# Kernel optimization log

Hardware: AMD Instinct MI355X
Metric: run time of the kernel (lower is better)

## Reference

```python
import jax, jax.numpy as jnp
import numpy as np

N_NODES = 50000
IN_CH = 128
N_EDGES = 800000
ADD_CONST = 0.5


def setup_inputs() -> dict:
    key = jax.random.key(0)
    k1, k2, k3, k4, k5 = jax.random.split(key, 5)
    x = jax.random.normal(k1, (N_NODES, IN_CH), dtype=jnp.float32)
    edge_index = jax.random.randint(k2, (2, N_EDGES), 0, N_NODES, dtype=jnp.int32)
    edge_weight = jax.random.uniform(k3, (N_EDGES,), dtype=jnp.float32)
    # Linear(2*C -> 1): split into source/target halves (mathematically identical
    # to Linear on concat([x[row], x[col]])). Xavier-uniform-ish scale.
    lim = float(np.sqrt(6.0 / (2 * IN_CH + 1)))
    w_src = jax.random.uniform(k4, (IN_CH,), minval=-lim, maxval=lim, dtype=jnp.float32)
    w_dst = jax.random.uniform(k5, (IN_CH,), minval=-lim, maxval=lim, dtype=jnp.float32)
    b = jnp.zeros((), dtype=jnp.float32)
    return {"x": x, "w_src": w_src, "w_dst": w_dst, "b": b,
            "edge_index": edge_index, "edge_weight": edge_weight}


def _normalize_edge_score(score, row, num_nodes):
    """Per-source-node softmax over strictly-positive scores, +0.5; nodes with
    no positive incident edge keep raw scores (faithful to torch loop)."""
    pos = score > 0
    has_pos = jax.ops.segment_max(pos.astype(jnp.int32), row, num_segments=num_nodes) > 0
    neg_big = jnp.asarray(jnp.finfo(score.dtype).min, score.dtype)
    smax = jax.ops.segment_max(jnp.where(pos, score, neg_big), row, num_segments=num_nodes)
    safe_max = jnp.where(has_pos, smax, 0.0)
    exp_s = jnp.where(pos, jnp.exp(score - safe_max[row]), 0.0)
    denom = jax.ops.segment_sum(exp_s, row, num_segments=num_nodes)
    denom = jnp.where(denom > 0, denom, 1.0)
    soft = jnp.where(pos, exp_s / denom[row] + ADD_CONST, 0.0)
    return jnp.where(has_pos[row], soft, score)


def reference(x, w_src, w_dst, b, edge_index, edge_weight):
    N = x.shape[0]
    row, col = edge_index[0], edge_index[1]

    # Edge score: Linear on concat([x[row], x[col]]) == per-node projections gathered.
    score = (x @ w_src)[row] + (x @ w_dst)[col] + b          # [E]
    norm = _normalize_edge_score(score, row, N)              # [E]

    # Greedy contraction in descending score order. Because the torch loop skips
    # any edge whose endpoint cluster already has size > 1, this is exactly a
    # greedy maximal matching: carry only a per-node 'matched' bitmask.
    perm = jnp.argsort(-norm)
    r_s, c_s, s_s = row[perm], col[perm], norm[perm]

    def step(matched, uv):
        u, v = uv
        ok = (u != v) & ~matched[u] & ~matched[v]
        matched = matched.at[u].set(matched[u] | ok)
        matched = matched.at[v].set(matched[v] | ok)
        return matched, ok

    _, sel = jax.lax.scan(step, jnp.zeros((N,), dtype=bool), (r_s, c_s))  # sel: [E]

    # cluster[v] = u for each selected edge (u, v); everything else identity.
    drop_v = jnp.where(sel, c_s, N)   # out-of-range indices are dropped
    drop_u = jnp.where(sel, r_s, N)
    cluster = jnp.arange(N, dtype=jnp.int32).at[drop_v].set(r_s, mode='drop')
    s_rep = jnp.ones((N,), x.dtype).at[drop_u].set(s_s, mode='drop')       # score of merging edge at rep u
    partner = jnp.arange(N, dtype=jnp.int32).at[drop_u].set(c_s, mode='drop')
    rep_sel = jnp.zeros((N,), bool).at[drop_u].set(True, mode='drop')

    # torch: merged_x[u] = (x[u] + x[v]) * s ; merged_x[v] stays x[v];
    # new_x = index_add by cluster  =>  rep u gets (x[u]+x[v])*s + x[v].
    sum_x = jax.ops.segment_sum(x, cluster, num_segments=N)               # [N, C]
    new_x = sum_x * s_rep[:, None] + jnp.where(rep_sel[:, None], x[partner], 0.0)

    counts = jax.ops.segment_sum(jnp.ones((N,), jnp.int32), cluster, num_segments=N)
    is_rep = counts > 0          # rows of new_x that correspond to surviving clusters

    # Remap edges to cluster representatives; self-loops masked out.
    new_row = cluster[row]
    new_col = cluster[col]
    edge_valid = new_row != new_col

    return new_x, cluster, is_rep, new_row, new_col, edge_valid, edge_weight
```

## Files before the change

kernel.cpp:

```cpp
#include <hip/hip_runtime.h>
#include <cmath>

#define IN_CH 128
#define NBUCK 128
#define LNMAX 392
#define PLW(p) __hip_atomic_load((p), __ATOMIC_RELAXED, __HIP_MEMORY_SCOPE_WORKGROUP)

typedef unsigned long long ull;
typedef ull  ull2 __attribute__((ext_vector_type(2)));
typedef float f4  __attribute__((ext_vector_type(4)));

__device__ __forceinline__ ull make_key(float norm, int e) {
    unsigned int b = __float_as_uint(norm);
    unsigned int asc = (b & 0x80000000u) ? ~b : (b | 0x80000000u);
    unsigned int desc = ~asc;
    return (((ull)desc) << 32) | (unsigned int)e;
}

__global__ void proj_kernel(const float* __restrict__ x, const float* __restrict__ w_src,
                            const float* __restrict__ w_dst, float* __restrict__ p,
                            float* __restrict__ q,
                            ull* __restrict__ wsuit,
                            int* __restrict__ cluster, int* __restrict__ partner,
                            float* __restrict__ s_rep, int* __restrict__ bump,
                            int* __restrict__ btail, int N) {
    int gtid = blockIdx.x * blockDim.x + threadIdx.x;
    if (gtid == 0) *bump = 0;
    if (gtid < NBUCK) btail[gtid] = 0;
    if (gtid < N) {
        wsuit[gtid]    = ~0ULL;
        cluster[gtid]  = gtid;
        partner[gtid]  = gtid;
        s_rep[gtid]    = 1.0f;
    }
    int wave = gtid >> 6;
    int lane = threadIdx.x & 63;
    if (wave >= N) return;
    float2 xv = ((const float2*)(x + (size_t)wave * IN_CH))[lane];
    float2 ws = ((const float2*)w_src)[lane];
    float2 wd = ((const float2*)w_dst)[lane];
    double ap = (double)xv.x * (double)ws.x + (double)xv.y * (double)ws.y;
    double aq = (double)xv.x * (double)wd.x + (double)xv.y * (double)wd.y;
    #pragma unroll
    for (int off = 32; off > 0; off >>= 1) {
        ap += __shfl_down(ap, off);
        aq += __shfl_down(aq, off);
    }
    if (lane == 0) { p[wave] = (float)ap; q[wave] = (float)aq; }
}

__global__ void score_kernel(const int* __restrict__ row, const int* __restrict__ col,
                             const float* __restrict__ p, const float* __restrict__ q,
                             const float* __restrict__ bptr, float* __restrict__ score,
                             int2* __restrict__ rc, int* __restrict__ btail,
                             unsigned int* __restrict__ bucket, int bcap, int E) {
    __shared__ int cnt[NBUCK];
    __shared__ int gbase[NBUCK];
    int e = blockIdx.x * blockDim.x + threadIdx.x;
    if (threadIdx.x < NBUCK) cnt[threadIdx.x] = 0;
    __syncthreads();
    bool inb = e < E;
    int u = 0, v = 0, l1 = -1, l2 = -1, h1 = 0, h2 = 0;
    unsigned int selfbit = 0;
    if (inb) {
        u = row[e]; v = col[e];
        rc[e] = make_int2(u, v);
        float s = p[u] + q[v] + bptr[0];
        score[e] = s;
        selfbit = (u == v) ? (1u << 30) : 0u;
        h1 = u & (NBUCK - 1); l1 = atomicAdd(&cnt[h1], 1);
        if (u != v) {
            h2 = v & (NBUCK - 1); l2 = atomicAdd(&cnt[h2], 1);
        }
    }
    __syncthreads();
    if (threadIdx.x < NBUCK) gbase[threadIdx.x] = atomicAdd(&btail[threadIdx.x], cnt[threadIdx.x]);
    __syncthreads();
    if (l1 >= 0) bucket[(size_t)h1 * bcap + gbase[h1] + l1] =
        (unsigned int)e | ((unsigned int)(u >> 7) << 21) | selfbit;
    if (l2 >= 0) bucket[(size_t)h2 * bcap + gbase[h2] + l2] =
        (unsigned int)e | (1u << 20) | ((unsigned int)(v >> 7) << 21);
}

__global__ void slot_kernel(unsigned int* __restrict__ bucket, const int* __restrict__ btail,
                            int bcap, const float* __restrict__ score,
                            unsigned int* __restrict__ node_max, double* __restrict__ denom,
                            int* __restrict__ bump, int2* __restrict__ seg, int N) {
    __shared__ int hist[LNMAX];
    __shared__ unsigned int maxv[LNMAX];
    __shared__ double dden[LNMAX];
    __shared__ int scan[512];
    __shared__ int basesh;
    int b = blockIdx.x;
    int t = threadIdx.x;
    for (int i = t; i < LNMAX; i += blockDim.x) {
        hist[i] = 0; maxv[i] = 0u; dden[i] = 0.0;
    }
    __syncthreads();
    int n = btail[b];
    unsigned int* bk = bucket + (size_t)b * bcap;
    for (int i = t; i < n; i += blockDim.x) {
        unsigned int ent = bk[i];
        if (!(ent & (1u << 20))) {
            int e = (int)(ent & 0xfffffu);
            float s = score[e];
            if (s > 0.0f) {
                int ln = (int)((ent >> 21) & 0x1ffu);
                atomicMax(&maxv[ln], __float_as_uint(s));
            }
        }
    }
    __syncthreads();
    for (int i = t; i < n; i += blockDim.x) {
        unsigned int ent = bk[i];
        int ln = (int)((ent >> 21) & 0x1ffu);
        if (!(ent & (1u << 20))) {
            unsigned int mb = maxv[ln];
            int e = (int)(ent & 0xfffffu);
            float s = score[e];
            if (mb != 0u && s > 0.0f) {
                float m = __uint_as_float(mb);
                float ev = (float)exp((double)(s - m));
                atomicAdd(&dden[ln], (double)ev);
            }
        }
        if (ent & (1u << 30)) {
            bk[i] = 0xFFFFFFFFu;
        } else {
            int slot = atomicAdd(&hist[ln], 1);
            bk[i] = (ent & 0x1fffffu) | ((unsigned int)slot << 21);
        }
    }
    __syncthreads();
    int node = (t << 7) | b;
    int d  = (t < LNMAX && node < N) ? hist[t] : 0;
    int pd = (d + 3) & ~3;
    scan[t] = pd;
    __syncthreads();
    #pragma unroll
    for (int off = 1; off < 512; off <<= 1) {
        int add = (t >= off) ? scan[t - off] : 0;
        __syncthreads();
        scan[t] += add;
        __syncthreads();
    }
    if (t == 511) basesh = atomicAdd(bump, scan[511]);
    __syncthreads();
    if (t < LNMAX && node < N) {
        int lo = basesh + scan[t] - pd;
        seg[node]      = make_int2(lo, lo + d);
        node_max[node] = maxv[t];
        denom[node]    = dden[t];
    }
}

__global__ void norm_key_kernel(const int* __restrict__ row, const float* __restrict__ score,
                                const unsigned int* __restrict__ node_max,
                                const double* __restrict__ denom, float* __restrict__ norm,
                                ull* __restrict__ keyn, int E) {
    int e = blockIdx.x * blockDim.x + threadIdx.x;
    if (e >= E) return;
    int u = row[e];
    unsigned int mb = node_max[u];
    float nv;
    if (mb != 0u) {
        float s = score[e];
        if (s > 0.0f) {
            float m = __uint_as_float(mb);
            float ev = (float)exp((double)(s - m));
            float d = (float)denom[u];
            nv = ev / d + 0.5f;
        } else {
            nv = 0.0f;
        }
    } else {
        nv = score[e];
    }
    norm[e] = nv;
    keyn[e] = make_key(nv, e);
}

__global__ void csr_scatter_kernel(const unsigned int* __restrict__ bucket,
                                   const int* __restrict__ btail, int bcap,
                                   const ull* __restrict__ keyn, const int2* __restrict__ rc,
                                   const int2* __restrict__ seg,
                                   ull2* __restrict__ adj, int bpx) {
    int xcd = blockIdx.x & 7;
    int sub = blockIdx.x >> 3;
    for (int bb = 0; bb < NBUCK / 8; ++bb) {
        int b = xcd + (bb << 3);
        int n = btail[b];
        const unsigned int* bk = bucket + (size_t)b * bcap;
        for (int i = sub * blockDim.x + threadIdx.x; i < n; i += bpx * blockDim.x) {
            unsigned int ent = bk[i];
            if (ent == 0xFFFFFFFFu) continue;
            int e    = (int)(ent & 0xfffffu);
            int side = (int)((ent >> 20) & 1u);
            int slot = (int)(ent >> 21);
            int2 pr = rc[e];
            int dst = side ? pr.y : pr.x;
            int nb  = side ? pr.x : pr.y;
            ull2 w; w.x = keyn[e]; w.y = (ull)nb;
            adj[seg[dst].x + slot] = w;
        }
    }
}

__global__ void suitor_kernel(const int2* __restrict__ seg,
                              const ull2* __restrict__ adj,
                              const int2* __restrict__ rc,
                              ull* __restrict__ ws, int N) {
    int grp  = (blockIdx.x * blockDim.x + threadIdx.x) >> 5;
    int lane = threadIdx.x & 31;
    if (grp >= N) return;
    int cur = grp;
    int2 lohi;
    ull excl = 0ULL;
    ull lk = ~0ULL;
    int lv = -1;
    bool reload = true;
    for (int guard = 0; guard < 1000000; ++guard) {
        if (reload) {
            lohi = seg[cur];
            excl = 0ULL;
            lk = ~0ULL; lv = -1;
            for (int i = lohi.x + lane; i < lohi.y; i += 32) {
                ull2 ent = adj[i];
                ull k = ent.x;
                if (k < lk) {
                    int v = (int)ent.y;
                    if (k < PLW(&ws[v])) { lk = k; lv = v; }
                }
            }
            reload = false;
        } else if (lk != ~0ULL && lk <= excl) {
            lk = ~0ULL; lv = -1;
            for (int i = lohi.x + lane; i < lohi.y; i += 32) {
                ull2 ent = adj[i];
                ull k = ent.x;
                if (k > excl && k < lk) {
                    int v = (int)ent.y;
                    if (k < PLW(&ws[v])) { lk = k; lv = v; }
                }
            }
        }
        ull bk = lk; int bv = lv;
        #pragma unroll
        for (int off = 16; off > 0; off >>= 1) {
            ull ok = __shfl_xor(bk, off, 32);
            int ov = __shfl_xor(bv, off, 32);
            if (ok < bk) { bk = ok; bv = ov; }
        }
        if (bk == ~0ULL) break;
        ull old;
        if (lane == 0) old = atomicMin(&ws[bv], bk);
        old = __shfl(old, 0, 32);
        if (old <= bk) {
            excl = bk;
            continue;
        }
        if (old == ~0ULL) break;
        int e = (int)(old & 0xffffffffu);
        int2 pr = rc[e];
        cur = pr.x ^ pr.y ^ bv;
        reload = true;
    }
}

__global__ void extract_kernel(const int2* __restrict__ rc, const float* __restrict__ norm,
                               const ull* __restrict__ ws,
                               int* __restrict__ cluster, int* __restrict__ partner,
                               float* __restrict__ s_rep, int N) {
    int w = blockIdx.x * blockDim.x + threadIdx.x;
    if (w >= N) return;
    ull k = ws[w];
    if (k == ~0ULL) return;
    int e = (int)(k & 0xffffffffu);
    int2 pr = rc[e];
    int a = pr.x, b = pr.y;
    if (w != a) return;
    if (ws[b] == k) {
        cluster[b] = a;
        partner[a] = b;
        s_rep[a]   = norm[e];
    }
}

__global__ void out_kernel(const float* __restrict__ x, const int* __restrict__ cluster,
                           const int* __restrict__ partner, const float* __restrict__ s_rep,
                           const int* __restrict__ row, const int* __restrict__ col,
                           const float* __restrict__ w,
                           float* __restrict__ out_newx, float* __restrict__ out_cluster,
                           float* __restrict__ out_isrep, float* __restrict__ out_nrow,
                           float* __restrict__ out_ncol, float* __restrict__ out_valid,
                           float* __restrict__ out_w, int N, int E, int NB1) {
    if ((int)blockIdx.x < NB1) {
        int t = blockIdx.x * blockDim.x + threadIdx.x;
        if (t >= N * (IN_CH / 4)) return;
        int n = t >> 5;
        int c = (t & 31) * 4;
        int cl = cluster[n];
        if ((t & 31) == 0) {
            out_cluster[n] = (float)cl;
            out_isrep[n]   = (cl == n) ? 1.0f : 0.0f;
        }
        f4 o;
        int v = partner[n];
        if (cl != n) {
            o = (f4)0.0f;
        } else if (v != n) {
            float s = s_rep[n];
            f4 xu = *(const f4*)(x + (size_t)n * IN_CH + c);
            f4 xv = *(const f4*)(x + (size_t)v * IN_CH + c);
            o = (xu + xv) * s + xv;
        } else {
            o = *(const f4*)(x + (size_t)n * IN_CH + c);
        }
        __builtin_nontemporal_store(o, (f4*)out_newx + t);
    } else {
        int e = (blockIdx.x - NB1) * blockDim.x + threadIdx.x;
        if (e >= E) return;
        int nr = cluster[row[e]];
        int nc = cluster[col[e]];
        out_nrow[e]  = (float)nr;
        out_ncol[e]  = (float)nc;
        out_valid[e] = (nr != nc) ? 1.0f : 0.0f;
        out_w[e]     = w[e];
    }
}

extern "C" void kernel_launch(void* const* d_in, const int* in_sizes, int n_in_args,
                              void* d_out, int out_size, void* d_ws, size_t ws_size,
                              hipStream_t stream) {
    const float* x     = (const float*)d_in[0];
    const float* w_src = (const float*)d_in[1];
    const float* w_dst = (const float*)d_in[2];
    const float* bptr  = (const float*)d_in[3];
    const int*   ei    = (const int*)d_in[4];
    const float* ew    = (const float*)d_in[5];
    const int N = in_sizes[0] / IN_CH;
    const int E = in_sizes[5];
    const int* row = ei;
    const int* col = ei + E;

    char* wsb = (char*)d_ws;
    size_t off = 0;
    auto alloc = [&](size_t bytes) -> void* {
        off = (off + 255) & ~(size_t)255;
        void* ptr = wsb + off;
        off += bytes;
        return ptr;
    };
    const int bcap = E / 64 + E / 512 + 1024;
    float*        score    = (float*)alloc((size_t)E * 4);
    float*        norm     = (float*)alloc((size_t)E * 4);
    int2*         rc       = (int2*)alloc((size_t)E * 8);
    ull*          keyn     = (ull*)alloc((size_t)E * 8);
    ull2*         adj      = (ull2*)alloc(((size_t)2 * E + 4 * N) * 16);
    unsigned int* bucket   = (unsigned int*)alloc((size_t)NBUCK * bcap * 4);
    unsigned int* node_max = (unsigned int*)alloc((size_t)N * 4);
    double*       denom    = (double*)alloc((size_t)N * 8);
    ull*          wsuit    = (ull*)alloc((size_t)N * 8);
    int2*         seg      = (int2*)alloc((size_t)N * 8);
    int*          cluster  = (int*)alloc((size_t)N * 4);
    int*          partner  = (int*)alloc((size_t)N * 4);
    float*        s_rep    = (float*)alloc((size_t)N * 4);
    float*        pbuf     = (float*)alloc((size_t)N * 4);
    float*        qbuf     = (float*)alloc((size_t)N * 4);
    int*          bump     = (int*)alloc(64);
    int*          btail    = (int*)alloc((size_t)NBUCK * 4);

    float* out       = (float*)d_out;
    float* o_newx    = out;
    float* o_cluster = out + (size_t)N * IN_CH;
    float* o_isrep   = o_cluster + N;
    float* o_nrow    = o_isrep + N;
    float* o_ncol    = o_nrow + E;
    float* o_valid   = o_ncol + E;
    float* o_w       = o_valid + E;

    const int T = 256;
    const int TS = 512;
    hipLaunchKernelGGL(proj_kernel, dim3((N * 64 + T - 1) / T), dim3(T), 0, stream,
                       x, w_src, w_dst, pbuf, qbuf,
                       wsuit, cluster, partner, s_rep, bump, btail, N);
    hipLaunchKernelGGL(score_kernel, dim3((E + TS - 1) / TS), dim3(TS), 0, stream,
                       row, col, pbuf, qbuf, bptr, score, rc,
                       btail, bucket, bcap, E);
    hipLaunchKernelGGL(slot_kernel, dim3(NBUCK), dim3(512), 0, stream,
                       bucket, btail, bcap, score, node_max, denom, bump, seg, N);
    hipLaunchKernelGGL(norm_key_kernel, dim3((E + T - 1) / T), dim3(T), 0, stream,
                       row, score, node_max, denom, norm, keyn, E);
    const int bpx = 40;
    hipLaunchKernelGGL(csr_scatter_kernel, dim3(8 * bpx), dim3(T), 0, stream,
                       bucket, btail, bcap, keyn, rc, seg, adj, bpx);
    hipLaunchKernelGGL(suitor_kernel, dim3((N * 32 + T - 1) / T), dim3(T), 0, stream,
                       seg, adj, rc, wsuit, N);
    hipLaunchKernelGGL(extract_kernel, dim3((N + T - 1) / T), dim3(T), 0, stream,
                       rc, norm, wsuit, cluster, partner, s_rep, N);
    const int NB1 = (N * 32 + T - 1) / T;
    const int NB2 = (E + T - 1) / T;
    hipLaunchKernelGGL(out_kernel, dim3(NB1 + NB2), dim3(T), 0, stream,
                       x, cluster, partner, s_rep, row, col, ew,
                       o_newx, o_cluster, o_isrep, o_nrow, o_ncol, o_valid, o_w, N, E, NB1);
    (void)ws_size; (void)out_size; (void)n_in_args;
}
```

Baseline: 356.0 us.

## Fuse edge normalization into CSR scatter and extract; remap suitor groups per XCD

Removes the separate norm_key kernel and its norm/keyn buffers. The normalized score and sort key are recomputed on the fly inside csr_scatter (via norm_of) and inside extract, which saves one launch and about 12 bytes per edge of writes and rereads. It also remaps which node each suitor wavefront handles, so that nodes are interleaved by blockIdx&7, apparently to spread each contiguous node range across the XCDs. The cost is an extra random read of node_max, denom and score per edge and a double-precision exp repeated in the scatter.

After: 367.1 us. +3.1%, slower.

```diff
diff --git a/kernel.cpp b/kernel.cpp
--- a/kernel.cpp
+++ b/kernel.cpp
@@ -15,6 +15,23 @@
     unsigned int asc = (b & 0x80000000u) ? ~b : (b | 0x80000000u);
     unsigned int desc = ~asc;
     return (((ull)desc) << 32) | (unsigned int)e;
+}
+
+__device__ __forceinline__ float norm_of(int e, int u, const float* __restrict__ score,
+                                         const unsigned int* __restrict__ node_max,
+                                         const double* __restrict__ denom) {
+    unsigned int mb = node_max[u];
+    float s = score[e];
+    if (mb != 0u) {
+        if (s > 0.0f) {
+            float m = __uint_as_float(mb);
+            float ev = (float)exp((double)(s - m));
+            float d = (float)denom[u];
+            return ev / d + 0.5f;
+        }
+        return 0.0f;
+    }
+    return s;
 }
 
 __global__ void proj_kernel(const float* __restrict__ x, const float* __restrict__ w_src,
@@ -154,35 +171,12 @@
     }
 }
 
-__global__ void norm_key_kernel(const int* __restrict__ row, const float* __restrict__ score,
-                                const unsigned int* __restrict__ node_max,
-                                const double* __restrict__ denom, float* __restrict__ norm,
-                                ull* __restrict__ keyn, int E) {
-    int e = blockIdx.x * blockDim.x + threadIdx.x;
-    if (e >= E) return;
-    int u = row[e];
-    unsigned int mb = node_max[u];
-    float nv;
-    if (mb != 0u) {
-        float s = score[e];
-        if (s > 0.0f) {
-            float m = __uint_as_float(mb);
-            float ev = (float)exp((double)(s - m));
-            float d = (float)denom[u];
-            nv = ev / d + 0.5f;
-        } else {
-            nv = 0.0f;
-        }
-    } else {
-        nv = score[e];
-    }
-    norm[e] = nv;
-    keyn[e] = make_key(nv, e);
-}
-
 __global__ void csr_scatter_kernel(const unsigned int* __restrict__ bucket,
                                    const int* __restrict__ btail, int bcap,
-                                   const ull* __restrict__ keyn, const int2* __restrict__ rc,
+                                   const float* __restrict__ score,
+                                   const unsigned int* __restrict__ node_max,
+                                   const double* __restrict__ denom,
+                                   const int2* __restrict__ rc,
                                    const int2* __restrict__ seg,
                                    ull2* __restrict__ adj, int bpx) {
     int xcd = blockIdx.x & 7;
@@ -200,7 +194,9 @@
             int2 pr = rc[e];
             int dst = side ? pr.y : pr.x;
             int nb  = side ? pr.x : pr.y;
-            ull2 w; w.x = keyn[e]; w.y = (ull)nb;
+            ull2 w;
+            w.x = make_key(norm_of(e, pr.x, score, node_max, denom), e);
+            w.y = (ull)nb;
             adj[seg[dst].x + slot] = w;
         }
     }
@@ -210,7 +206,9 @@
                               const ull2* __restrict__ adj,
                               const int2* __restrict__ rc,
                               ull* __restrict__ ws, int N) {
-    int grp  = (blockIdx.x * blockDim.x + threadIdx.x) >> 5;
+    int lg   = threadIdx.x >> 5;
+    int b    = blockIdx.x;
+    int grp  = ((((b >> 3) << 3) + lg) << 3) | (b & 7);
     int lane = threadIdx.x & 31;
     if (grp >= N) return;
     int cur = grp;
@@ -267,7 +265,10 @@
     }
 }
 
-__global__ void extract_kernel(const int2* __restrict__ rc, const float* __restrict__ norm,
+__global__ void extract_kernel(const int2* __restrict__ rc,
+                               const float* __restrict__ score,
+                               const unsigned int* __restrict__ node_max,
+                               const double* __restrict__ denom,
                                const ull* __restrict__ ws,
                                int* __restrict__ cluster, int* __restrict__ partner,
                                float* __restrict__ s_rep, int N) {
@@ -282,7 +283,7 @@
     if (ws[b] == k) {
         cluster[b] = a;
         partner[a] = b;
-        s_rep[a]   = norm[e];
+        s_rep[a]   = norm_of(e, a, score, node_max, denom);
     }
 }
 
@@ -353,9 +354,7 @@
     };
     const int bcap = E / 64 + E / 512 + 1024;
     float*        score    = (float*)alloc((size_t)E * 4);
-    float*        norm     = (float*)alloc((size_t)E * 4);
     int2*         rc       = (int2*)alloc((size_t)E * 8);
-    ull*          keyn     = (ull*)alloc((size_t)E * 8);
     ull2*         adj      = (ull2*)alloc(((size_t)2 * E + 4 * N) * 16);
     unsigned int* bucket   = (unsigned int*)alloc((size_t)NBUCK * bcap * 4);
     unsigned int* node_max = (unsigned int*)alloc((size_t)N * 4);
@@ -389,15 +388,14 @@
                        btail, bucket, bcap, E);
     hipLaunchKernelGGL(slot_kernel, dim3(NBUCK), dim3(512), 0, stream,
                        bucket, btail, bcap, score, node_max, denom, bump, seg, N);
-    hipLaunchKernelGGL(norm_key_kernel, dim3((E + T - 1) / T), dim3(T), 0, stream,
-                       row, score, node_max, denom, norm, keyn, E);
     const int bpx = 40;
     hipLaunchKernelGGL(csr_scatter_kernel, dim3(8 * bpx), dim3(T), 0, stream,
-                       bucket, btail, bcap, keyn, rc, seg, adj, bpx);
-    hipLaunchKernelGGL(suitor_kernel, dim3((N * 32 + T - 1) / T), dim3(T), 0, stream,
+                       bucket, btail, bcap, score, node_max, denom, rc, seg, adj, bpx);
+    const int SB = ((N + 63) / 64) * 8;
+    hipLaunchKernelGGL(suitor_kernel, dim3(SB), dim3(T), 0, stream,
                        seg, adj, rc, wsuit, N);
     hipLaunchKernelGGL(extract_kernel, dim3((N + T - 1) / T), dim3(T), 0, stream,
-                       rc, norm, wsuit, cluster, partner, s_rep, N);
+                       rc, score, node_max, denom, wsuit, cluster, partner, s_rep, N);
     const int NB1 = (N * 32 + T - 1) / T;
     const int NB2 = (E + T - 1) / T;
     hipLaunchKernelGGL(out_kernel, dim3(NB1 + NB2), dim3(T), 0, stream,
```
